# Performance work log

Hardware: AMD Instinct MI355X
Metric: run time of the kernel (lower is better)

The kernel has to match this reference:

```python
import jax, jax.numpy as jnp
import numpy as np

G = 256                       # points form a jittered G x G grid -> N = 65536
H = 0.01                      # particle spacing
PARTICLE_RADIUS = 0.0025      # init kwarg
RADIUS = 5.0 * PARTICLE_RADIUS  # filter_extent / 2 = ball-query radius
EPS = 1e-12


def _ball_to_cube_xy(rel):
    # Open3D 'ball_to_cube_volume_preserving': sphere->cylinder->cube.
    # Returns the (u, v) cube coordinates; z kernel dim has size 1 so w is unused.
    x, y, z = rel[..., 0], rel[..., 1], rel[..., 2]
    sq = x * x + y * y + z * z
    norm = jnp.sqrt(jnp.maximum(sq, EPS))
    rxy2 = x * x + y * y
    rxy = jnp.sqrt(jnp.maximum(rxy2, EPS))
    cond = 1.25 * z * z > rxy2
    s1 = jnp.sqrt(3.0 * norm / jnp.maximum(norm + jnp.abs(z), EPS))
    s2 = norm / rxy
    cx = jnp.where(cond, x * s1, x * s2)
    cy = jnp.where(cond, y * s1, y * s2)
    nz = sq > EPS
    cx = jnp.where(nz, cx, 0.0)
    cy = jnp.where(nz, cy, 0.0)
    # cylinder -> cube: area-preserving disc -> square on (cx, cy)
    r = jnp.sqrt(jnp.maximum(cx * cx + cy * cy, EPS))
    condx = jnp.abs(cx) >= jnp.abs(cy)
    dx = jnp.where(jnp.abs(cx) > 1e-9, cx, 1.0)
    dy = jnp.where(jnp.abs(cy) > 1e-9, cy, 1.0)
    fop = 4.0 / np.pi
    u = jnp.where(condx, jnp.sign(cx) * r,
                  jnp.sign(cy) * r * fop * jnp.arctan(cx / dy))
    v = jnp.where(condx, jnp.sign(cx) * r * fop * jnp.arctan(cy / dx),
                  jnp.sign(cy) * r)
    small = (cx * cx + cy * cy) <= EPS
    return jnp.where(small, 0.0, u), jnp.where(small, 0.0, v)


def _cconv(feats, W, b, pos3, nbr_idx, nbr_mask):
    # ContinuousConv: kernel_size=[4,4,1], align_corners, linear interpolation,
    # poly6 window, normalize=False. Single z plane -> pure bilinear over 4x4 taps.
    rel = (pos3[nbr_idx] - pos3[:, None, :]) / RADIUS          # (N,K,3)
    r2 = jnp.sum(rel * rel, axis=-1)                           # (N,K)
    win = jnp.clip((1.0 - jnp.clip(r2, 0.0, 1.0)) ** 3, 0.0, 1.0)
    win = win * ((r2 <= 1.0) & nbr_mask).astype(feats.dtype)
    u, v = _ball_to_cube_xy(rel)
    gx = jnp.clip((u + 1.0) * 0.5 * 3.0, 0.0, 3.0)             # align_corners coord
    gy = jnp.clip((v + 1.0) * 0.5 * 3.0, 0.0, 3.0)
    grid = jnp.arange(4, dtype=feats.dtype)
    wx = jnp.maximum(1.0 - jnp.abs(gx[..., None] - grid), 0.0)  # (N,K,4)
    wy = jnp.maximum(1.0 - jnp.abs(gy[..., None] - grid), 0.0)  # (N,K,4)
    wfull = (wx[..., :, None] * wy[..., None, :]).reshape(wx.shape[0], wx.shape[1], 16)
    wfull = wfull * win[..., None]                             # (N,K,16)
    fN = feats[nbr_idx]                                        # (N,K,Cin)
    t = jnp.einsum('nkg,nkc->ngc', wfull, fN)                  # (N,16,Cin)
    Wf = W.reshape(16, W.shape[2], W.shape[3])
    return jnp.einsum('ngc,gcd->nd', t, Wf) + b


def _forward(pos, vel, nbr_idx, nbr_mask, bn_gamma, bn_beta,
             conv_ws, conv_bs, dense_ws, dense_bs):
    zcol = jnp.zeros((pos.shape[0], 1), pos.dtype)
    pos3 = jnp.concatenate([pos, zcol], axis=1)
    vel3 = jnp.concatenate([vel, zcol], axis=1)
    # BatchNorm1d(3) in training mode (biased batch statistics, eps=1e-5)
    m = vel3.mean(axis=0)
    var = jnp.mean((vel3 - m) ** 2, axis=0)
    feats_in = bn_gamma * (vel3 - m) * jax.lax.rsqrt(var + 1e-5) + bn_beta
    c0 = _cconv(feats_in, conv_ws[0], conv_bs[0], pos3, nbr_idx, nbr_mask)
    d0 = feats_in @ dense_ws[0] + dense_bs[0]
    f = jnp.concatenate([c0, d0], axis=-1)                     # (N,64)
    for i in range(1, 5):
        inp = jax.nn.relu(f)
        c = _cconv(inp, conv_ws[i], conv_bs[i], pos3, nbr_idx, nbr_mask)
        d = inp @ dense_ws[i] + dense_bs[i]
        f = c + d + f if d.shape[-1] == f.shape[-1] else c + d
    return jnp.tanh(f) * 0.8 + 1.0


def setup_inputs() -> dict:
    key = jax.random.key(0)
    ks = jax.random.split(key, 32)
    N = G * G
    ii, jj = np.meshgrid(np.arange(G), np.arange(G), indexing='ij')
    base = np.stack([ii, jj], -1).reshape(-1, 2).astype(np.float32) * H
    jit_ = jax.random.uniform(ks[0], (N, 2), minval=-0.2 * H, maxval=0.2 * H)
    pos = jnp.asarray(base) + jit_
    vel = jax.random.normal(ks[1], (N, 2), dtype=jnp.float32)
    # fixed 3x3 stencil candidates; true ball query done by distance mask in-conv
    nbrs, masks = [], []
    for di in (-1, 0, 1):
        for dj in (-1, 0, 1):
            ni, nj = ii + di, jj + dj
            valid = (ni >= 0) & (ni < G) & (nj >= 0) & (nj < G)
            nbrs.append((np.clip(ni, 0, G - 1) * G + np.clip(nj, 0, G - 1)).reshape(-1))
            masks.append(valid.reshape(-1))
    nbr_idx = jnp.asarray(np.stack(nbrs, 1).astype(np.int32))
    nbr_mask = jnp.asarray(np.stack(masks, 1))
    io = [(3, 32), (64, 64), (64, 128), (128, 256), (256, 1)]
    inp = {'pos': pos, 'vel': vel, 'nbr_idx': nbr_idx, 'nbr_mask': nbr_mask,
           'bn_gamma': jnp.ones(3, jnp.float32), 'bn_beta': jnp.zeros(3, jnp.float32)}
    for i, (ci, co) in enumerate(io):
        s = 0.1 / np.sqrt(3.0 * ci)
        inp[f'conv_w{i}'] = jax.random.normal(ks[2 + i], (4, 4, ci, co), dtype=jnp.float32) * s
        inp[f'conv_b{i}'] = jnp.zeros(co, jnp.float32)
        b = 1.0 / np.sqrt(ci)
        inp[f'dense_w{i}'] = jax.random.uniform(ks[10 + i], (ci, co), minval=-b, maxval=b, dtype=jnp.float32)
        inp[f'dense_b{i}'] = jax.random.uniform(ks[20 + i], (co,), minval=-b, maxval=b, dtype=jnp.float32)
    return inp


def reference(pos, vel, nbr_idx, nbr_mask, bn_gamma, bn_beta,
              conv_w0, conv_b0, conv_w1, conv_b1, conv_w2, conv_b2,
              conv_w3, conv_b3, conv_w4, conv_b4,
              dense_w0, dense_b0, dense_w1, dense_b1, dense_w2, dense_b2,
              dense_w3, dense_b3, dense_w4, dense_b4):
    conv_ws = [conv_w0, conv_w1, conv_w2, conv_w3, conv_w4]
    conv_bs = [conv_b0, conv_b1, conv_b2, conv_b3, conv_b4]
    dense_ws = [dense_w0, dense_w1, dense_w2, dense_w3, dense_w4]
    dense_bs = [dense_b0, dense_b1, dense_b2, dense_b3, dense_b4]
    return _forward(pos, vel, nbr_idx, nbr_mask, bn_gamma, bn_beta,
                    conv_ws, conv_bs, dense_ws, dense_bs)
```

## Files before the change

kernel.cpp:

```cpp
#include <hip/hip_runtime.h>
#include <hip/hip_bf16.h>
#include <cstdint>


#define GRIDW 256
#define NPTS  65536
#define RADI  0.0125f
#define EPSF  1e-12f

typedef unsigned short ushort_t;
typedef unsigned int   uint_t;
typedef __attribute__((ext_vector_type(8))) short short8;
typedef __attribute__((ext_vector_type(4))) float f32x4;
typedef __attribute__((ext_vector_type(2))) float f32x2;

template<int N> struct IC { static constexpr int v = N; };

__device__ __forceinline__ float bf2f(ushort_t h){
  union { uint_t u; float f; } c; c.u = ((uint_t)h) << 16; return c.f;
}
__device__ __forceinline__ ushort_t f2bf(float f){
  union { float f; uint_t u; } c; c.f = f;
  uint_t u = c.u;
  u += 0x7fffu + ((u >> 16) & 1u);
  return (ushort_t)(u >> 16);
}
__device__ __forceinline__ uint_t cvtpk(float a, float b){
  uint_t r; asm("v_cvt_pk_bf16_f32 %0, %1, %2" : "=v"(r) : "v"(a), "v"(b)); return r;
}
__device__ __forceinline__ void pkfma_lo(f32x2& d, f32x2 t, f32x2 v){
  asm("v_pk_fma_f32 %0, %1, %2, %0 op_sel:[0,0,0] op_sel_hi:[1,0,1]"
      : "+v"(d) : "v"(t), "v"(v));
}
__device__ __forceinline__ void pkfma_hi(f32x2& d, f32x2 t, f32x2 v){
  asm("v_pk_fma_f32 %0, %1, %2, %0 op_sel:[0,1,0] op_sel_hi:[1,1,1]"
      : "+v"(d) : "v"(t), "v"(v));
}
__device__ __forceinline__ int swz(int row, int byteoff){
  return row*64 + ((((byteoff >> 4) ^ ((row >> 1) & 3)) & 3) << 4) + (byteoff & 15);
}

__global__ __launch_bounds__(256) void bn_partial(const float2* __restrict__ vel,
                                                  float* __restrict__ part){
  __shared__ float s[256][4];
  const int t = threadIdx.x;
  const int id = blockIdx.x * 256 + t;
  float2 v = vel[id];
  s[t][0] = v.x; s[t][1] = v.y; s[t][2] = v.x * v.x; s[t][3] = v.y * v.y;
  __syncthreads();
  for (int off = 128; off > 0; off >>= 1){
    if (t < off){
      s[t][0] += s[t+off][0]; s[t][1] += s[t+off][1];
      s[t][2] += s[t+off][2]; s[t][3] += s[t+off][3];
    }
    __syncthreads();
  }
  if (t == 0){
    part[blockIdx.x*4+0] = s[0][0]; part[blockIdx.x*4+1] = s[0][1];
    part[blockIdx.x*4+2] = s[0][2]; part[blockIdx.x*4+3] = s[0][3];
  }
}

__global__ __launch_bounds__(256) void bn_final(const float* __restrict__ part,
                                                const float* __restrict__ gamma,
                                                const float* __restrict__ beta,
                                                float* __restrict__ stats){
  __shared__ float s[256][4];
  const int t = threadIdx.x;
  const float4 p = reinterpret_cast<const float4*>(part)[t];
  s[t][0] = p.x; s[t][1] = p.y; s[t][2] = p.z; s[t][3] = p.w;
  __syncthreads();
  for (int off = 128; off > 0; off >>= 1){
    if (t < off){
      s[t][0] += s[t+off][0]; s[t][1] += s[t+off][1];
      s[t][2] += s[t+off][2]; s[t][3] += s[t+off][3];
    }
    __syncthreads();
  }
  if (t == 0){
    const float invN = 1.0f / 65536.0f;
    float m0 = s[0][0]*invN, m1 = s[0][1]*invN;
    float var0 = s[0][2]*invN - m0*m0;
    float var1 = s[0][3]*invN - m1*m1;
    float A0 = gamma[0] * rsqrtf(var0 + 1e-5f);
    float A1 = gamma[1] * rsqrtf(var1 + 1e-5f);
    stats[0] = A0; stats[1] = beta[0] - A0*m0;
    stats[2] = A1; stats[3] = beta[1] - A1*m1;
    stats[4] = beta[2];
  }
}

__global__ __launch_bounds__(256) void feats_kernel(const float2* __restrict__ vel,
                                                    const float* __restrict__ stats,
                                                    float4* __restrict__ fin){
  const int id = blockIdx.x * 256 + threadIdx.x;
  float2 v = vel[id];
  float A0 = stats[0], B0 = stats[1], A1 = stats[2], B1 = stats[3], C2 = stats[4];
  fin[id] = make_float4(A0*v.x + B0, A1*v.y + B1, C2, 0.0f);
}

__global__ __launch_bounds__(256) void geo_kernel(const float2* __restrict__ pos,
                                                  float4* __restrict__ wgeo){
  const int id = blockIdx.x * 256 + threadIdx.x;
  const int n = id / 9;
  const int k = id - n * 9;
  const int i = n >> 8, j = n & 255;
  const int di = k / 3 - 1, dj = k - (k/3)*3 - 1;
  const int ni = i + di, nj = j + dj;
  const bool valid = (ni >= 0) && (ni < GRIDW) && (nj >= 0) && (nj < GRIDW);
  const int mi = min(max(ni, 0), GRIDW-1), mj = min(max(nj, 0), GRIDW-1);
  const int m = (mi << 8) | mj;
  float2 pn = pos[n], pm = pos[m];
  float x = (pm.x - pn.x) * (1.0f / RADI);
  float y = (pm.y - pn.y) * (1.0f / RADI);
  float sq = x*x + y*y;
  bool nz = sq > EPSF;
  float cx = nz ? x : 0.0f;
  float cy = nz ? y : 0.0f;
  float rr = cx*cx + cy*cy;
  float r = sqrtf(fmaxf(rr, EPSF));
  float acx = fabsf(cx), acy = fabsf(cy);
  bool condx = acx >= acy;
  float dx  = (acx > 1e-9f) ? cx : 1.0f;
  float dyv = (acy > 1e-9f) ? cy : 1.0f;
  const float fop = 1.27323954473516268615f;
  float sx = (cx > 0.f) ? 1.f : ((cx < 0.f) ? -1.f : 0.f);
  float sy = (cy > 0.f) ? 1.f : ((cy < 0.f) ? -1.f : 0.f);
  float u, v;
  if (condx){ u = sx * r;                    v = sx * r * fop * atanf(cy/dx); }
  else      { u = sy * r * fop * atanf(cx/dyv); v = sy * r; }
  if (rr <= EPSF){ u = 0.0f; v = 0.0f; }
  float gx = fminf(fmaxf((u + 1.0f) * 1.5f, 0.0f), 3.0f);
  float gy = fminf(fmaxf((v + 1.0f) * 1.5f, 0.0f), 3.0f);
  float pw = 1.0f - fminf(fmaxf(sq, 0.0f), 1.0f);
  float win = pw * pw * pw;
  win = (sq <= 1.0f && valid) ? win : 0.0f;
  wgeo[id] = make_float4(win, gx, gy, 0.0f);
}

template<int Cin, int Cout>
__global__ __launch_bounds__(256) void wprep(const float* __restrict__ cw,
                                             const float* __restrict__ dw,
                                             ushort_t* __restrict__ Wf){
  constexpr int G = Cout/16;
  const int id = blockIdx.x*256 + threadIdx.x;
  const int ch = id / (G*64);
  const int r  = id - ch*G*64;
  const int grp = r >> 6, l = r & 63;
  const int d  = grp*16 + (l & 15);
  const int kb = ch*32 + (l >> 4)*8;
  ushort_t o[8];
  #pragma unroll
  for (int e = 0; e < 8; ++e){
    const int kk = kb + e;
    float v;
    if (kk < 16*Cin){ int c = kk >> 4, g = kk & 15; v = cw[(size_t)(g*Cin + c)*Cout + d]; }
    else v = dw[(size_t)(kk - 16*Cin)*Cout + d];
    o[e] = f2bf(v);
  }
  *reinterpret_cast<uint4*>(Wf + (size_t)id*8) = *reinterpret_cast<uint4*>(o);
}

__global__ __launch_bounds__(256) void layer0_kernel(
    const float4* __restrict__ fin, const float4* __restrict__ wgeo,
    const float* __restrict__ cw, const float* __restrict__ cb,
    const float* __restrict__ dw, const float* __restrict__ db,
    ushort_t* __restrict__ f0){
  __shared__ float Wc[48*32];
  __shared__ float Wd[96];
  __shared__ float Bs[64];
  const int tid = threadIdx.x;
  for (int idx = tid; idx < 1536; idx += 256) Wc[idx] = cw[idx];
  if (tid < 96) Wd[tid] = dw[tid];
  if (tid < 32){ Bs[tid] = cb[tid]; Bs[32+tid] = db[tid]; }
  __syncthreads();
  const int p = tid >> 3, q = tid & 7;
  const int n = blockIdx.x * 32 + p;
  const int i = n >> 8, j = n & 255;
  float A[48];
  #pragma unroll
  for (int a = 0; a < 48; ++a) A[a] = 0.0f;
  const float4 fc = fin[n];
  #pragma unroll
  for (int k = 0; k < 9; ++k){
    const int di = k/3 - 1, dj = k - (k/3)*3 - 1;
    const int mi = min(max(i+di,0),255), mj = min(max(j+dj,0),255);
    const int m = (mi << 8) | mj;
    float4 geo = wgeo[n*9 + k];
    float4 fm = fin[m];
    float wx[4], wy[4];
    #pragma unroll
    for (int a = 0; a < 4; ++a){
      wx[a] = fmaxf(1.0f - fabsf(geo.y - (float)a), 0.0f);
      wy[a] = fmaxf(1.0f - fabsf(geo.z - (float)a), 0.0f);
    }
    #pragma unroll
    for (int ix = 0; ix < 4; ++ix)
      #pragma unroll
      for (int iy = 0; iy < 4; ++iy){
        float w = geo.x * wx[ix] * wy[iy];
        int g = ix*4 + iy;
        A[g*3+0] += w * fm.x; A[g*3+1] += w * fm.y; A[g*3+2] += w * fm.z;
      }
  }
  if (q < 4){
    #pragma unroll
    for (int jj = 0; jj < 8; ++jj){
      int d = q*8 + jj;
      float acc = Bs[d];
      #pragma unroll
      for (int a = 0; a < 48; ++a) acc += A[a] * Wc[a*32 + d];
      f0[n*64 + d] = f2bf(acc);
    }
  } else {
    #pragma unroll
    for (int jj = 0; jj < 8; ++jj){
      int d2 = (q-4)*8 + jj;
      float acc = Bs[32+d2] + fc.x*Wd[0*32+d2] + fc.y*Wd[1*32+d2] + fc.z*Wd[2*32+d2];
      f0[n*64 + 32 + d2] = f2bf(acc);
    }
  }
}

template<int Cin, int Cout, bool RESID>
__global__ __launch_bounds__(256) void conv_mfma(
    const ushort_t* __restrict__ fin, const float4* __restrict__ wgeo,
    const ushort_t* __restrict__ Wf,
    const float* __restrict__ cb, const float* __restrict__ db,
    ushort_t* __restrict__ fout){
  constexpr int K   = 17*Cin;
  constexpr int NCC = Cin/2;
  constexpr int NCH = K/32;
  constexpr int HSTR = 137;
  constexpr int G   = Cout/16;
  constexpr int MF  = 4;
  constexpr int NF  = Cout/64;

  __shared__ f32x2 halo64[16*HSTR];
  __shared__ __align__(16) ushort_t A_lds[2][64*32];

  const int tid = threadIdx.x;
  const int i0 = (blockIdx.x >> 3) * 2;
  const int j0 = (blockIdx.x & 7) * 32;

  auto stage = [&](int ph){
    for (int idx = tid; idx < 544; idx += 256){
      const int loc = idx >> 2, c8l = idx & 3;
      const int r = loc / 34, col = loc - r*34;
      const int gi = min(max(i0 - 1 + r, 0), 255);
      const int gj = min(max(j0 - 1 + col, 0), 255);
      const int mm = (gi << 8) | gj;
      uint4 v = *reinterpret_cast<const uint4*>(fin + (size_t)mm*Cin + ph*32 + c8l*8);
      const uint_t* vp = (const uint_t*)&v;
      #pragma unroll
      for (int q = 0; q < 4; ++q){
        uint_t u = vp[q];
        f32x2 f;
        f.x = fmaxf(__uint_as_float(u << 16), 0.0f);
        f.y = fmaxf(__uint_as_float(u & 0xFFFF0000u), 0.0f);
        halo64[(c8l*4 + q)*HSTR + loc] = f;
      }
    }
  };

  const int m  = tid & 63;
  const int gq = tid >> 6;
  const int g0 = gq * 4;
  const int n_m = ((i0 + (m >> 5)) << 8) + j0 + (m & 31);
  const int lane = m;
  const int lr = lane & 15, lg = lane >> 4;
  const int ctr = (1 + (m >> 5))*34 + 1 + (m & 31);

  stage(0);
  f32x2 tap2[9][2];
  #pragma unroll
  for (int k = 0; k < 9; ++k){
    float4 geo = wgeo[(size_t)n_m*9 + k];
    float wxg = fmaxf(1.0f - fabsf(geo.y - (float)gq), 0.0f);
    float s = geo.x * wxg;
    tap2[k][0].x = s * fmaxf(1.0f - fabsf(geo.z - 0.0f), 0.0f);
    tap2[k][0].y = s * fmaxf(1.0f - fabsf(geo.z - 1.0f), 0.0f);
    tap2[k][1].x = s * fmaxf(1.0f - fabsf(geo.z - 2.0f), 0.0f);
    tap2[k][1].y = s * fmaxf(1.0f - fabsf(geo.z - 3.0f), 0.0f);
  }

  const int Nbase = gq * (NF*16);

  int aoff[MF];
  #pragma unroll
  for (int mi = 0; mi < MF; ++mi) aoff[mi] = swz(mi*16 + lr, lg*16);
  const int s0 = swz(m, 2*g0);
  const int s1 = swz(m, 32 + 2*g0);
  const int sd = swz(m, gq*16);

  const ushort_t* wp = Wf + (size_t)(gq*NF)*512 + lane*8;

  f32x4 acc[MF][NF];
  #pragma unroll
  for (int a = 0; a < MF; ++a)
    #pragma unroll
    for (int b = 0; b < NF; ++b) acc[a][b] = (f32x4){0.f,0.f,0.f,0.f};

  short8 bfrA[NF], bfrB[NF];
  auto loadB = [&](short8 (&dst)[NF], int ch){
    const ushort_t* wpc = wp + (size_t)ch * (G*512);
    #pragma unroll
    for (int ni = 0; ni < NF; ++ni)
      dst[ni] = *reinterpret_cast<const short8*>(wpc + ni*512);
  };

  auto buildA = [&](auto BC, int ch){
    constexpr int B = decltype(BC)::v;
    char* Ab = (char*)A_lds[B];
    if (ch < NCC){
      const f32x2* hb = &halo64[(ch & 15)*HSTR + ctr - 35];
      f32x2 a01 = {0.f,0.f}, a23 = {0.f,0.f};
      f32x2 b01 = {0.f,0.f}, b23 = {0.f,0.f};
      #pragma unroll
      for (int kr = 0; kr < 3; ++kr)
        #pragma unroll
        for (int kc = 0; kc < 3; ++kc){
          const f32x2 val = hb[kr*34 + kc];
          const int k = kr*3 + kc;
          pkfma_lo(a01, tap2[k][0], val);
          pkfma_lo(a23, tap2[k][1], val);
          pkfma_hi(b01, tap2[k][0], val);
          pkfma_hi(b23, tap2[k][1], val);
        }
      uint2 plo, phi;
      plo.x = cvtpk(a01.x, a01.y); plo.y = cvtpk(a23.x, a23.y);
      phi.x = cvtpk(b01.x, b01.y); phi.y = cvtpk(b23.x, b23.y);
      *reinterpret_cast<uint2*>(Ab + s0) = plo;
      *reinterpret_cast<uint2*>(Ab + s1) = phi;
    } else {
      const int cd0 = (ch - NCC)*32 + gq*8;
      uint4 u = *reinterpret_cast<const uint4*>(fin + (size_t)n_m*Cin + cd0);
      uint_t* up = (uint_t*)&u;
      #pragma unroll
      for (int q = 0; q < 4; ++q){
        uint_t w = up[q];
        uint_t lo = (w & 0x00008000u) ? 0u : (w & 0x0000FFFFu);
        uint_t hi = (w & 0x80000000u) ? 0u : (w & 0xFFFF0000u);
        up[q] = hi | lo;
      }
      *reinterpret_cast<uint4*>(Ab + sd) = u;
    }
  };

  auto domfma = [&](short8 (&af)[MF], short8 (&bfr)[NF]){
    #pragma unroll
    for (int mi = 0; mi < MF; ++mi)
      #pragma unroll
      for (int ni = 0; ni < NF; ++ni)
        acc[mi][ni] = __builtin_amdgcn_mfma_f32_16x16x32_bf16(
            af[mi], bfr[ni], acc[mi][ni], 0, 0, 0);
  };

  auto body = [&](auto BC, int ch, bool prep){
    constexpr int B = decltype(BC)::v;
    __syncthreads();
    if (prep){
      if constexpr (B == 0) loadB(bfrB, ch + 1);
      else                  loadB(bfrA, ch + 1);
    }
    short8 af[MF];
    const char* Ab = (const char*)A_lds[B];
    #pragma unroll
    for (int mi = 0; mi < MF; ++mi)
      af[mi] = *reinterpret_cast<const short8*>(Ab + aoff[mi]);
    if (prep) buildA(IC<B^1>{}, ch + 1);
    if constexpr (B == 0) domfma(af, bfrA);
    else                  domfma(af, bfrB);
  };

  __syncthreads();
  loadB(bfrA, 0);
  buildA(IC<0>{}, 0);

  for (int ch2 = 0; ch2 < NCH; ch2 += 2){
    body(IC<0>{}, ch2, true);
    const int nxt = ch2 + 2;
    if ((nxt < NCC) && ((nxt & 15) == 0)){ __syncthreads(); stage(nxt >> 4); }
    body(IC<1>{}, ch2 + 1, nxt < NCH);
  }

  float bias[NF];
  #pragma unroll
  for (int ni = 0; ni < NF; ++ni){
    const int d = Nbase + ni*16 + lr;
    bias[ni] = cb[d] + db[d];
  }
  #pragma unroll
  for (int mi = 0; mi < MF; ++mi){
    #pragma unroll
    for (int r = 0; r < 4; ++r){
      const int row = mi*16 + lg*4 + r;
      const int n = ((i0 + (row >> 5)) << 8) + j0 + (row & 31);
      #pragma unroll
      for (int ni = 0; ni < NF; ++ni){
        const int d = Nbase + ni*16 + lr;
        float v = acc[mi][ni][r] + bias[ni];
        if (RESID) v += bf2f(fin[(size_t)n*Cin + d]);
        fout[(size_t)n*Cout + d] = f2bf(v);
      }
    }
  }
}

__global__ __launch_bounds__(256) void layer4a_kernel(
    const ushort_t* __restrict__ f3, const float* __restrict__ cw4,
    const float* __restrict__ dw4, float* __restrict__ y){
  __shared__ float Wy[17*256];
  __shared__ float red[4*1088];
  const int tid = threadIdx.x;
  for (int idx = tid; idx < 4096; idx += 256) Wy[idx] = cw4[idx];
  Wy[4096 + tid] = dw4[tid];
  __syncthreads();
  const int m = tid & 63, q = tid >> 6;
  const int n = blockIdx.x * 64 + m;
  const float4* Wy4 = reinterpret_cast<const float4*>(Wy);
  float acc[17];
  #pragma unroll
  for (int g = 0; g < 17; ++g) acc[g] = 0.0f;
  const uint4* frow = reinterpret_cast<const uint4*>(f3 + (size_t)n*256 + q*64);
  #pragma unroll
  for (int it = 0; it < 8; ++it){
    uint4 hv = frow[it];
    const uint_t* up = (const uint_t*)&hv;
    float f[8];
    #pragma unroll
    for (int w = 0; w < 4; ++w){
      uint_t u = up[w];
      f[2*w+0] = (u & 0x00008000u) ? 0.0f : __uint_as_float(u << 16);
      f[2*w+1] = (u & 0x80000000u) ? 0.0f : __uint_as_float(u & 0xFFFF0000u);
    }
    const int i4 = q*16 + it*2;
    #pragma unroll
    for (int g = 0; g < 17; ++g){
      float4 w0 = Wy4[g*64 + i4];
      float4 w1 = Wy4[g*64 + i4 + 1];
      acc[g] += w0.x*f[0] + w0.y*f[1] + w0.z*f[2] + w0.w*f[3]
              + w1.x*f[4] + w1.y*f[5] + w1.z*f[6] + w1.w*f[7];
    }
  }
  #pragma unroll
  for (int g = 0; g < 17; ++g) red[q*1088 + m*17 + g] = acc[g];
  __syncthreads();
  for (int idx = tid; idx < 1088; idx += 256){
    const int g = idx >> 6, mm = idx & 63;
    float s = red[0*1088 + mm*17 + g] + red[1*1088 + mm*17 + g]
            + red[2*1088 + mm*17 + g] + red[3*1088 + mm*17 + g];
    y[g*65536 + blockIdx.x*64 + mm] = s;
  }
}

__global__ __launch_bounds__(256) void layer4b_kernel(
    const float4* __restrict__ wgeo, const float* __restrict__ y,
    const float* __restrict__ cb4, const float* __restrict__ db4,
    float* __restrict__ out){
  const int n = blockIdx.x * 256 + threadIdx.x;
  const int i = n >> 8, j = n & 255;
  float acc = cb4[0] + db4[0] + y[16*65536 + n];
  #pragma unroll
  for (int k = 0; k < 9; ++k){
    const int di = k/3 - 1, dj = k - (k/3)*3 - 1;
    const int mi = min(max(i+di,0),255), mj = min(max(j+dj,0),255);
    const int m = (mi << 8) | mj;
    float4 geo = wgeo[n*9 + k];
    float wx[4], wy[4];
    #pragma unroll
    for (int a = 0; a < 4; ++a){
      wx[a] = fmaxf(1.0f - fabsf(geo.y - (float)a), 0.0f);
      wy[a] = fmaxf(1.0f - fabsf(geo.z - (float)a), 0.0f);
    }
    float s = 0.0f;
    #pragma unroll
    for (int ix = 0; ix < 4; ++ix){
      float sy = 0.0f;
      #pragma unroll
      for (int iy = 0; iy < 4; ++iy) sy += wy[iy] * y[(ix*4 + iy)*65536 + m];
      s += wx[ix] * sy;
    }
    acc += geo.x * s;
  }
  out[n] = tanhf(acc) * 0.8f + 1.0f;
}

extern "C" void kernel_launch(void* const* d_in, const int* in_sizes, int n_in,
                              void* d_out, int out_size, void* d_ws, size_t ws_size,
                              hipStream_t stream){
  const float* pos = (const float*)d_in[0];
  const float* vel = (const float*)d_in[1];
  const float* bng = (const float*)d_in[4];
  const float* bnb = (const float*)d_in[5];
  const bool dict = (in_sizes[8] == 96);
  const float *cwp[5], *cbp[5], *dwp[5], *dbp[5];
  for (int l = 0; l < 5; ++l){
    if (dict){
      cwp[l] = (const float*)d_in[6 + 4*l]; cbp[l] = (const float*)d_in[7 + 4*l];
      dwp[l] = (const float*)d_in[8 + 4*l]; dbp[l] = (const float*)d_in[9 + 4*l];
    } else {
      cwp[l] = (const float*)d_in[6 + 2*l];  cbp[l] = (const float*)d_in[7 + 2*l];
      dwp[l] = (const float*)d_in[16 + 2*l]; dbp[l] = (const float*)d_in[17 + 2*l];
    }
  }
  char* wsb = (char*)d_ws;
  float*    part  = (float*)   (wsb + 0);
  float*    stats = (float*)   (wsb + 4096);
  float4*   fin   = (float4*)  (wsb + 8192);
  float4*   wgeo  = (float4*)  (wsb + 1056768);
  ushort_t* Wt1   = (ushort_t*)(wsb + 10493952);
  ushort_t* Wt2   = (ushort_t*)(wsb + 10633216);
  ushort_t* Wt3   = (ushort_t*)(wsb + 10911744);
  ushort_t* f0    = (ushort_t*)(wsb + 12025856);
  ushort_t* f1    = (ushort_t*)(wsb + 20414464);
  ushort_t* f2    = (ushort_t*)(wsb + 28803072);
  ushort_t* f3    = (ushort_t*)(wsb + 45580288);
  float*    y     = (float*)   (wsb + 12025856);
  float*    outp  = (float*)d_out;

  hipLaunchKernelGGL(bn_partial, dim3(256), dim3(256), 0, stream, (const float2*)vel, part);
  hipLaunchKernelGGL(bn_final, dim3(1), dim3(256), 0, stream, part, bng, bnb, stats);
  hipLaunchKernelGGL(feats_kernel, dim3(256), dim3(256), 0, stream, (const float2*)vel, stats, fin);
  hipLaunchKernelGGL(geo_kernel, dim3(2304), dim3(256), 0, stream, (const float2*)pos, wgeo);
  hipLaunchKernelGGL((wprep<64,64>),   dim3(34),  dim3(256), 0, stream, cwp[1], dwp[1], Wt1);
  hipLaunchKernelGGL((wprep<64,128>),  dim3(68),  dim3(256), 0, stream, cwp[2], dwp[2], Wt2);
  hipLaunchKernelGGL((wprep<128,256>), dim3(272), dim3(256), 0, stream, cwp[3], dwp[3], Wt3);
  hipLaunchKernelGGL(layer0_kernel, dim3(2048), dim3(256), 0, stream,
                     fin, wgeo, cwp[0], cbp[0], dwp[0], dbp[0], f0);
  hipLaunchKernelGGL((conv_mfma<64,64,true>),   dim3(1024), dim3(256), 0, stream,
                     f0, wgeo, Wt1, cbp[1], dbp[1], f1);
  hipLaunchKernelGGL((conv_mfma<64,128,false>), dim3(1024), dim3(256), 0, stream,
                     f1, wgeo, Wt2, cbp[2], dbp[2], f2);
  hipLaunchKernelGGL((conv_mfma<128,256,false>),dim3(1024), dim3(256), 0, stream,
                     f2, wgeo, Wt3, cbp[3], dbp[3], f3);
  hipLaunchKernelGGL(layer4a_kernel, dim3(1024), dim3(256), 0, stream, f3, cwp[4], dwp[4], y);
  hipLaunchKernelGGL(layer4b_kernel, dim3(256), dim3(256), 0, stream, wgeo, y, cbp[4], dbp[4], outp);
}
```

Before: 238.3 us.

## Use 8-wave conv MFMA kernel for the 128-to-256 layer

```diff
diff --git a/kernel.cpp b/kernel.cpp
--- a/kernel.cpp
+++ b/kernel.cpp
@@ -407,6 +407,194 @@
   }
 }
 
+template<int Cin, int Cout, bool RESID>
+__global__ __launch_bounds__(512) void conv_mfma8(
+    const ushort_t* __restrict__ fin, const float4* __restrict__ wgeo,
+    const ushort_t* __restrict__ Wf,
+    const float* __restrict__ cb, const float* __restrict__ db,
+    ushort_t* __restrict__ fout){
+  constexpr int K   = 17*Cin;
+  constexpr int NCC = Cin/2;
+  constexpr int NCH = K/32;
+  constexpr int HSTR = 137;
+  constexpr int G   = Cout/16;
+  constexpr int MF  = 4;
+  constexpr int NF  = Cout/128;
+
+  __shared__ f32x2 halo64[16*HSTR];
+  __shared__ __align__(16) ushort_t A_lds[2][64*32];
+
+  const int tid = threadIdx.x;
+  const int i0 = (blockIdx.x >> 3) * 2;
+  const int j0 = (blockIdx.x & 7) * 32;
+
+  auto stage = [&](int ph){
+    for (int idx = tid; idx < 544; idx += 512){
+      const int loc = idx >> 2, c8l = idx & 3;
+      const int r = loc / 34, col = loc - r*34;
+      const int gi = min(max(i0 - 1 + r, 0), 255);
+      const int gj = min(max(j0 - 1 + col, 0), 255);
+      const int mm = (gi << 8) | gj;
+      uint4 v = *reinterpret_cast<const uint4*>(fin + (size_t)mm*Cin + ph*32 + c8l*8);
+      const uint_t* vp = (const uint_t*)&v;
+      #pragma unroll
+      for (int q = 0; q < 4; ++q){
+        uint_t u = vp[q];
+        f32x2 f;
+        f.x = fmaxf(__uint_as_float(u << 16), 0.0f);
+        f.y = fmaxf(__uint_as_float(u & 0xFFFF0000u), 0.0f);
+        halo64[(c8l*4 + q)*HSTR + loc] = f;
+      }
+    }
+  };
+
+  const int m  = tid & 63;
+  const int wv = tid >> 6;
+  const int gq = wv & 3;
+  const int cl = wv >> 2;
+  const int g0 = gq * 4;
+  const int n_m = ((i0 + (m >> 5)) << 8) + j0 + (m & 31);
+  const int lane = m;
+  const int lr = lane & 15, lg = lane >> 4;
+  const int ctr = (1 + (m >> 5))*34 + 1 + (m & 31);
+
+  stage(0);
+  f32x2 tap2[9][2];
+  #pragma unroll
+  for (int k = 0; k < 9; ++k){
+    float4 geo = wgeo[(size_t)n_m*9 + k];
+    float wxg = fmaxf(1.0f - fabsf(geo.y - (float)gq), 0.0f);
+    float s = geo.x * wxg;
+    tap2[k][0].x = s * fmaxf(1.0f - fabsf(geo.z - 0.0f), 0.0f);
+    tap2[k][0].y = s * fmaxf(1.0f - fabsf(geo.z - 1.0f), 0.0f);
+    tap2[k][1].x = s * fmaxf(1.0f - fabsf(geo.z - 2.0f), 0.0f);
+    tap2[k][1].y = s * fmaxf(1.0f - fabsf(geo.z - 3.0f), 0.0f);
+  }
+
+  const int Nbase = wv * (NF*16);
+
+  int aoff[MF];
+  #pragma unroll
+  for (int mi = 0; mi < MF; ++mi) aoff[mi] = swz(mi*16 + lr, lg*16);
+  const int sc  = swz(m, cl*32 + gq*8);
+  const int sdn = swz(m, wv*8);
+
+  const ushort_t* wp = Wf + (size_t)(wv*NF)*512 + lane*8;
+
+  f32x4 acc[MF][NF];
+  #pragma unroll
+  for (int a = 0; a < MF; ++a)
+    #pragma unroll
+    for (int b = 0; b < NF; ++b) acc[a][b] = (f32x4){0.f,0.f,0.f,0.f};
+
+  auto loadB = [&](short8 (&dst)[NF], int ch){
+    const ushort_t* wpc = wp + (size_t)ch * (G*512);
+    #pragma unroll
+    for (int ni = 0; ni < NF; ++ni)
+      dst[ni] = *reinterpret_cast<const short8*>(wpc + ni*512);
+  };
+
+  auto buildA = [&](auto BC, int ch){
+    constexpr int B = decltype(BC)::v;
+    char* Ab = (char*)A_lds[B];
+    if (ch < NCC){
+      const f32x2* hb = &halo64[(ch & 15)*HSTR + ctr - 35];
+      f32x2 a01 = {0.f,0.f}, a23 = {0.f,0.f};
+      if (cl == 0){
+        #pragma unroll
+        for (int kr = 0; kr < 3; ++kr)
+          #pragma unroll
+          for (int kc = 0; kc < 3; ++kc){
+            const f32x2 val = hb[kr*34 + kc];
+            const int k = kr*3 + kc;
+            pkfma_lo(a01, tap2[k][0], val);
+            pkfma_lo(a23, tap2[k][1], val);
+          }
+      } else {
+        #pragma unroll
+        for (int kr = 0; kr < 3; ++kr)
+          #pragma unroll
+          for (int kc = 0; kc < 3; ++kc){
+            const f32x2 val = hb[kr*34 + kc];
+            const int k = kr*3 + kc;
+            pkfma_hi(a01, tap2[k][0], val);
+            pkfma_hi(a23, tap2[k][1], val);
+          }
+      }
+      uint2 p;
+      p.x = cvtpk(a01.x, a01.y); p.y = cvtpk(a23.x, a23.y);
+      *reinterpret_cast<uint2*>(Ab + sc) = p;
+    } else {
+      const int cd0 = (ch - NCC)*32 + wv*4;
+      uint2 u = *reinterpret_cast<const uint2*>(fin + (size_t)n_m*Cin + cd0);
+      uint_t* up = (uint_t*)&u;
+      #pragma unroll
+      for (int q = 0; q < 2; ++q){
+        uint_t w = up[q];
+        uint_t lo = (w & 0x00008000u) ? 0u : (w & 0x0000FFFFu);
+        uint_t hi = (w & 0x80000000u) ? 0u : (w & 0xFFFF0000u);
+        up[q] = hi | lo;
+      }
+      *reinterpret_cast<uint2*>(Ab + sdn) = u;
+    }
+  };
+
+  auto domfma = [&](short8 (&af)[MF], short8 (&bfr)[NF]){
+    #pragma unroll
+    for (int mi = 0; mi < MF; ++mi)
+      #pragma unroll
+      for (int ni = 0; ni < NF; ++ni)
+        acc[mi][ni] = __builtin_amdgcn_mfma_f32_16x16x32_bf16(
+            af[mi], bfr[ni], acc[mi][ni], 0, 0, 0);
+  };
+
+  auto body = [&](auto BC, int ch, bool prep){
+    constexpr int B = decltype(BC)::v;
+    __syncthreads();
+    short8 bfr[NF];
+    loadB(bfr, ch);
+    short8 af[MF];
+    const char* Ab = (const char*)A_lds[B];
+    #pragma unroll
+    for (int mi = 0; mi < MF; ++mi)
+      af[mi] = *reinterpret_cast<const short8*>(Ab + aoff[mi]);
+    if (prep) buildA(IC<B^1>{}, ch + 1);
+    domfma(af, bfr);
+  };
+
+  __syncthreads();
+  buildA(IC<0>{}, 0);
+
+  for (int ch2 = 0; ch2 < NCH; ch2 += 2){
+    body(IC<0>{}, ch2, true);
+    const int nxt = ch2 + 2;
+    if ((nxt < NCC) && ((nxt & 15) == 0)){ __syncthreads(); stage(nxt >> 4); }
+    body(IC<1>{}, ch2 + 1, nxt < NCH);
+  }
+
+  float bias[NF];
+  #pragma unroll
+  for (int ni = 0; ni < NF; ++ni){
+    const int d = Nbase + ni*16 + lr;
+    bias[ni] = cb[d] + db[d];
+  }
+  #pragma unroll
+  for (int mi = 0; mi < MF; ++mi){
+    #pragma unroll
+    for (int r = 0; r < 4; ++r){
+      const int row = mi*16 + lg*4 + r;
+      const int n = ((i0 + (row >> 5)) << 8) + j0 + (row & 31);
+      #pragma unroll
+      for (int ni = 0; ni < NF; ++ni){
+        const int d = Nbase + ni*16 + lr;
+        float v = acc[mi][ni][r] + bias[ni];
+        if (RESID) v += bf2f(fin[(size_t)n*Cin + d]);
+        fout[(size_t)n*Cout + d] = f2bf(v);
+      }
+    }
+  }
+}
+
 __global__ __launch_bounds__(256) void layer4a_kernel(
     const ushort_t* __restrict__ f3, const float* __restrict__ cw4,
     const float* __restrict__ dw4, float* __restrict__ y){
@@ -532,7 +720,7 @@
                      f0, wgeo, Wt1, cbp[1], dbp[1], f1);
   hipLaunchKernelGGL((conv_mfma<64,128,false>), dim3(1024), dim3(256), 0, stream,
                      f1, wgeo, Wt2, cbp[2], dbp[2], f2);
-  hipLaunchKernelGGL((conv_mfma<128,256,false>),dim3(1024), dim3(256), 0, stream,
+  hipLaunchKernelGGL((conv_mfma8<128,256,false>),dim3(1024), dim3(512), 0, stream,
                      f2, wgeo, Wt3, cbp[3], dbp[3], f3);
   hipLaunchKernelGGL(layer4a_kernel, dim3(1024), dim3(256), 0, stream, f3, cwp[4], dwp[4], y);
   hipLaunchKernelGGL(layer4b_kernel, dim3(256), dim3(256), 0, stream, wgeo, y, cbp[4], dbp[4], outp);
```

New measurement: 247.9 us. 1.04x slower.
